# Kernel optimization log

Measured on AMD Instinct MI355X. Metric: run time of the kernel, lower is better.

The kernel has to match this reference:

```python
import jax, jax.numpy as jnp
import numpy as np

OPS_SIZE = (40, 40, 40)
ALPHA = 0.005
BETA = 0.01


def _disp_from_landmarks(coords, values):
    # coords, values: (N,3). Returns (3, W0, H0, D0) coarse displacement field.
    D0, H0, W0 = OPS_SIZE
    axes = [jnp.linspace(-1.0, 1.0, s) for s in OPS_SIZE]
    grid = jnp.stack(jnp.meshgrid(*axes, indexing='ij'), -1).reshape(-1, 3)  # (G,3)
    # squared distance ||g - c||^2 via expansion (avoids (N,G,3) repeat tensor)
    d2 = (jnp.sum(grid * grid, -1)[:, None]
          + jnp.sum(coords * coords, -1)[None, :]
          - 2.0 * grid @ coords.T)  # (G,N)
    w = jnp.exp(-d2 / ALPHA)
    w = (BETA + 1.0) * w / (jnp.sum(w, axis=1, keepdims=True) + BETA)
    disp = (w @ values).reshape(D0, H0, W0, 3)
    return jnp.transpose(disp, (3, 2, 1, 0))  # torch permute(3,2,1,0)


def _interp_axis(x, axis, out_s):
    # 1D linear resize along `axis`, matching F.interpolate align_corners=False
    in_s = x.shape[axis]
    c = jnp.maximum((jnp.arange(out_s, dtype=jnp.float32) + 0.5) * (in_s / out_s) - 0.5, 0.0)
    i0 = jnp.minimum(jnp.floor(c).astype(jnp.int32), in_s - 1)
    i1 = jnp.minimum(i0 + 1, in_s - 1)
    t = (c - i0.astype(jnp.float32)).astype(x.dtype)
    shp = [1] * x.ndim
    shp[axis] = out_s
    t = t.reshape(shp)
    return jnp.take(x, i0, axis=axis) * (1 - t) + jnp.take(x, i1, axis=axis) * t


def _resize_trilinear(x, out_size):
    # x: (C, d, h, w) -> (C, D, H, W); trilinear resize is separable
    for ax, s in zip((1, 2, 3), out_size):
        x = _interp_axis(x, ax, s)
    return x


def _grid_sample_3d(vol, grid):
    # vol: (B,C,D,H,W), grid: (B,Do,Ho,Wo,3), grid[...,0]=x indexes W.
    # mode='bilinear' (trilinear), padding_mode='zeros', align_corners=False
    B, C, D, H, W = vol.shape
    x = ((grid[..., 0] + 1.0) * W - 1.0) / 2.0
    y = ((grid[..., 1] + 1.0) * H - 1.0) / 2.0
    z = ((grid[..., 2] + 1.0) * D - 1.0) / 2.0

    def per_batch(v, x, y, z):
        x0 = jnp.floor(x); y0 = jnp.floor(y); z0 = jnp.floor(z)
        fx = x - x0; fy = y - y0; fz = z - z0
        x0i = x0.astype(jnp.int32); y0i = y0.astype(jnp.int32); z0i = z0.astype(jnp.int32)
        acc = jnp.zeros((C,) + x.shape, v.dtype)
        for dz in (0, 1):
            wz = fz if dz else 1.0 - fz
            zi = z0i + dz
            for dy in (0, 1):
                wy = fy if dy else 1.0 - fy
                yi = y0i + dy
                for dx in (0, 1):
                    wx = fx if dx else 1.0 - fx
                    xi = x0i + dx
                    m = ((zi >= 0) & (zi < D) & (yi >= 0) & (yi < H) & (xi >= 0) & (xi < W)).astype(v.dtype)
                    zc = jnp.clip(zi, 0, D - 1); yc = jnp.clip(yi, 0, H - 1); xc = jnp.clip(xi, 0, W - 1)
                    acc = acc + v[:, zc, yc, xc] * ((wz * wy * wx * m)[None])
        return acc

    return jax.vmap(per_batch)(vol, x, y, z)


def reference(orgin_mask, control_points_coords, control_points_offsets):
    B, C, D, H, W = orgin_mask.shape
    coords = control_points_coords + control_points_offsets  # (B,N,3)
    vals = -control_points_offsets                            # (B,N,3)
    disp = jax.vmap(_disp_from_landmarks)(coords, vals)       # (B,3,W0,H0,D0)
    flow = jax.vmap(lambda d: _resize_trilinear(d, (D, H, W)))(disp)  # (B,3,D,H,W)
    axes = [jnp.linspace(-1.0, 1.0, s) for s in (D, H, W)]
    base = jnp.stack(jnp.meshgrid(*axes, indexing='ij'), 0)   # (3,D,H,W)
    base = jnp.transpose(base, (0, 3, 2, 1))                  # torch permute(0,1,4,3,2); needs D==H==W
    warped = base[None] + flow                                # (B,3,D,H,W)
    warped = jnp.transpose(warped, (0, 2, 3, 4, 1))           # (B,D,H,W,3)
    return _grid_sample_3d(orgin_mask, warped)


def setup_inputs() -> dict:
    key = jax.random.key(0)
    k1, k2, k3 = jax.random.split(key, 3)
    orgin_mask = jax.random.uniform(k1, (2, 1, 128, 128, 128), dtype=jnp.float32)
    control_points_coords = jax.random.uniform(k2, (2, 1024, 3), dtype=jnp.float32, minval=-1.0, maxval=1.0)
    control_points_offsets = jax.random.normal(k3, (2, 1024, 3), dtype=jnp.float32) * 0.05
    return {"orgin_mask": orgin_mask,
            "control_points_coords": control_points_coords,
            "control_points_offsets": control_points_offsets}
```

## Files before the change

kernel.cpp:

```cpp
#include <hip/hip_runtime.h>
#include <math.h>

#define NLM   1024
#define NB    2
#define OPS   40
#define DIM   128
#define OPS3  (OPS*OPS*OPS)
#define DIM3  (DIM*DIM*DIM)

#define P_T 4
#define Q_T 4
#define R_T 8
#define NP  (OPS/P_T)
#define NQ  (OPS/Q_T)
#define NR  (OPS/R_T)
#define MARGIN 0.30f

#define K2f  (-288.5390081777927f)
#define M2f  ( 577.0780163555854f)


__device__ __forceinline__ float fexp2(float x) {
#if __has_builtin(__builtin_amdgcn_exp2f)
    return __builtin_amdgcn_exp2f(x);
#else
    return exp2f(x);
#endif
}

__global__ __launch_bounds__(128)
void coarse_kernel(const float* __restrict__ coords, const float* __restrict__ offs,
                   float4* __restrict__ C) {
    __shared__ float4 sA[NLM];
    __shared__ float4 sV[NLM];
    __shared__ int sCnt;

    const int t = threadIdx.x;
    const int b = blockIdx.y;
    const int tile = blockIdx.x;
    const int tp = tile / (NQ*NR);
    const int tq = (tile / NR) % NQ;
    const int tr = tile % NR;

    const float step = 2.f / (OPS - 1);
    const float bx0 = -1.f + step * (tr*R_T)          - MARGIN;
    const float bx1 = -1.f + step * (tr*R_T + R_T-1)  + MARGIN;
    const float by0 = -1.f + step * (tq*Q_T)          - MARGIN;
    const float by1 = -1.f + step * (tq*Q_T + Q_T-1)  + MARGIN;
    const float bz0 = -1.f + step * (tp*P_T)          - MARGIN;
    const float bz1 = -1.f + step * (tp*P_T + P_T-1)  + MARGIN;

    if (t == 0) sCnt = 0;
    __syncthreads();

    for (int n = t; n < NLM; n += 128) {
        const float* cp = coords + (b*NLM + n)*3;
        const float* op = offs   + (b*NLM + n)*3;
        float ox = op[0], oy = op[1], oz = op[2];
        float cx = cp[0] + ox, cy = cp[1] + oy, cz = cp[2] + oz;
        if (cx >= bx0 && cx <= bx1 && cy >= by0 && cy <= by1 &&
            cz >= bz0 && cz <= bz1) {
            int idx = atomicAdd(&sCnt, 1);
            sA[idx] = make_float4(cx, cy, cz, K2f*(cx*cx + cy*cy + cz*cz));
            sV[idx] = make_float4(-ox, -oy, -oz, 0.f);
        }
    }
    __syncthreads();
    const int cnt = sCnt;

    const int lp = t >> 5;
    const int lq = (t >> 3) & 3;
    const int lr = t & 7;
    const float gx = -1.f + step * (tr*R_T + lr);
    const float gy = -1.f + step * (tq*Q_T + lq);
    const float gz = -1.f + step * (tp*P_T + lp);
    const float h  = K2f * (gx*gx + gy*gy + gz*gz);

    float aS = 0.f, aX = 0.f, aY = 0.f, aZ = 0.f;
    for (int n = 0; n < cnt; ++n) {
        float4 a = sA[n];
        float4 v = sV[n];
        float u   = fmaf(gx, a.x, fmaf(gy, a.y, gz*a.z));
        float arg = fmaf(M2f, u, h + a.w);
        float e   = fexp2(arg);
        aS += e;
        aX = fmaf(e, v.x, aX);
        aY = fmaf(e, v.y, aY);
        aZ = fmaf(e, v.z, aZ);
    }

    const int p = tp*P_T + lp, q = tq*Q_T + lq, r = tr*R_T + lr;
    const float inv = 1.01f / (aS + 0.01f);
    C[b*OPS3 + (p*OPS + q)*OPS + r] = make_float4(aX*inv, aY*inv, aZ*inv, 0.f);
}

__device__ __forceinline__ void axis_interp(int t, int& a0, int& a1, float& w) {
    float c = fmaxf(0.3125f * (float)t - 0.34375f, 0.f);
    float f = floorf(c);
    a0 = (int)f;
    a1 = min(a0 + 1, OPS - 1);
    w = c - f;
}

__device__ __forceinline__ float4 lerp4(float4 a, float4 b, float t) {
    return make_float4(a.x + t*(b.x - a.x),
                       a.y + t*(b.y - a.y),
                       a.z + t*(b.z - a.z),
                       0.f);
}

typedef float vf2 __attribute__((ext_vector_type(2)));
struct __attribute__((packed, aligned(4))) P2 { vf2 v; };
__device__ __forceinline__ vf2 load2(const float* p) {
    return ((const P2*)p)->v;
}

struct AW {
    int r0, r1, r2, r3, xs;
    float e0, e1, wy0, wy1, wz0, wz1;
};

__device__ __forceinline__ AW make_aw(float px, float py, float pz) {
    AW s;
    float xf = floorf(px), yf = floorf(py), zf = floorf(pz);
    int x0 = (int)xf, y0 = (int)yf, z0 = (int)zf;
    float ax = px - xf, ay = py - yf, az = pz - zf;

    float wx0 = ((unsigned)x0     < 128u) ? (1.f - ax) : 0.f;
    float wx1 = ((unsigned)(x0+1) < 128u) ? ax         : 0.f;
    s.wy0 = ((unsigned)y0     < 128u) ? (1.f - ay) : 0.f;
    s.wy1 = ((unsigned)(y0+1) < 128u) ? ay         : 0.f;
    s.wz0 = ((unsigned)z0     < 128u) ? (1.f - az) : 0.f;
    s.wz1 = ((unsigned)(z0+1) < 128u) ? az         : 0.f;

    s.xs = min(max(x0, 0), 126);
    int d = x0 - s.xs;
    s.e0 = (d == 0) ? wx0 : ((d == -1) ? wx1 : 0.f);
    s.e1 = (d == 0) ? wx1 : ((d ==  1) ? wx0 : 0.f);

    int ya = (y0 & 127) << 7, yb2 = ((y0+1) & 127) << 7;
    int za = (z0 & 127) << 14, zb2 = ((z0+1) & 127) << 14;
    s.r0 = za + ya;  s.r1 = za + yb2;
    s.r2 = zb2 + ya; s.r3 = zb2 + yb2;
    return s;
}

__global__ __launch_bounds__(256)
void warp_kernel(const float* __restrict__ mask, const float4* __restrict__ C,
                 float* __restrict__ out) {
    __shared__ float4 sF[4][OPS];

    const int g = blockIdx.x;
    const int w = threadIdx.x >> 6;
    const int lane = threadIdx.x & 63;
    const int line = ((g & 7) << 12) + ((g >> 3) << 2) + w;
    const int j = line & (DIM-1);
    const int i = (line >> 7) & (DIM-1);
    const int b = line >> 14;

    int i0,i1,j0,j1; float ti,tj;
    axis_interp(i, i0, i1, ti);
    axis_interp(j, j0, j1, tj);

    const float4* Cb = C + b*OPS3;
    if (lane < OPS) {
        float4 c00 = Cb[(i0*OPS + j0)*OPS + lane];
        float4 c01 = Cb[(i0*OPS + j1)*OPS + lane];
        float4 c10 = Cb[(i1*OPS + j0)*OPS + lane];
        float4 c11 = Cb[(i1*OPS + j1)*OPS + lane];
        sF[w][lane] = lerp4(lerp4(c00, c01, tj), lerp4(c10, c11, tj), ti);
    }

    const float* M = mask + b * DIM3;
    const float s127 = 2.f / (DIM - 1);
    const float yb = -1.f + s127 * (float)j;
    const float zb = -1.f + s127 * (float)i;

    AW aw[2];
    #pragma unroll
    for (int c = 0; c < 2; ++c) {
        const int k = lane + (c << 6);
        int k0,k1; float tk;
        axis_interp(k, k0, k1, tk);
        float4 fl = lerp4(sF[w][k0], sF[w][k1], tk);
        float x = -1.f + s127 * (float)k + fl.x;
        float y = yb + fl.y;
        float z = zb + fl.z;
        aw[c] = make_aw(((x + 1.f) * (float)DIM - 1.f) * 0.5f,
                        ((y + 1.f) * (float)DIM - 1.f) * 0.5f,
                        ((z + 1.f) * (float)DIM - 1.f) * 0.5f);
    }

    vf2 t0[4], t1[4];
    {
        const AW& s = aw[0];
        t0[0] = load2(M + s.r0 + s.xs);
        t0[1] = load2(M + s.r1 + s.xs);
        t0[2] = load2(M + s.r2 + s.xs);
        t0[3] = load2(M + s.r3 + s.xs);
    }
    {
        const AW& s = aw[1];
        t1[0] = load2(M + s.r0 + s.xs);
        t1[1] = load2(M + s.r1 + s.xs);
        t1[2] = load2(M + s.r2 + s.xs);
        t1[3] = load2(M + s.r3 + s.xs);
    }

    float res[2];
    #pragma unroll
    for (int c = 0; c < 2; ++c) {
        const AW& s = aw[c];
        const vf2* tv = c ? t1 : t0;
        float w00 = s.wz0*s.wy0, w01 = s.wz0*s.wy1;
        float w10 = s.wz1*s.wy0, w11 = s.wz1*s.wy1;
        float r;
        r = tv[0].x * (w00*s.e0);
        r = fmaf(tv[0].y, w00*s.e1, r);
        r = fmaf(tv[1].x, w01*s.e0, r);
        r = fmaf(tv[1].y, w01*s.e1, r);
        r = fmaf(tv[2].x, w10*s.e0, r);
        r = fmaf(tv[2].y, w10*s.e1, r);
        r = fmaf(tv[3].x, w11*s.e0, r);
        r = fmaf(tv[3].y, w11*s.e1, r);
        res[c] = r;
    }
    out[(line << 7) + lane]      = res[0];
    out[(line << 7) + lane + 64] = res[1];
}

extern "C" void kernel_launch(void* const* d_in, const int* in_sizes, int n_in,
                              void* d_out, int out_size, void* d_ws, size_t ws_size,
                              hipStream_t stream) {
    const float* mask   = (const float*)d_in[0];
    const float* coords = (const float*)d_in[1];
    const float* offs   = (const float*)d_in[2];
    float* out = (float*)d_out;

    float4* coarse = (float4*)d_ws;

    dim3 g1(NP*NQ*NR, NB);
    coarse_kernel<<<g1, 128, 0, stream>>>(coords, offs, coarse);

    warp_kernel<<<NB*DIM*DIM/4, 256, 0, stream>>>(mask, coarse, out);
}
```

Measured before the change: 97.98 us.

## Stage per-wave bounding box of mask rows in LDS before trilinear gather

For each half-line, the wave reduces its min/max z, y and x sample indices with shuffles. If the bounding box fits, it copies those mask rows into shared memory with coalesced loads and gathers the eight corners from LDS. Otherwise it falls back to direct global gathers. The goal is to replace scattered 8-byte global loads with coalesced row copies, at the cost of wave reductions, extra LDS traffic and a serial copy loop.

Result: slower. 123.9 us (+26.5%).

```diff
diff --git a/kernel.cpp b/kernel.cpp
--- a/kernel.cpp
+++ b/kernel.cpp
@@ -18,6 +18,9 @@
 
 #define K2f  (-288.5390081777927f)
 #define M2f  ( 577.0780163555854f)
+
+#define ROWS_MAX 20
+#define NX_MAX   96
 
 
 __device__ __forceinline__ float fexp2(float x) {
@@ -116,7 +119,7 @@
 }
 
 struct AW {
-    int r0, r1, r2, r3, xs;
+    int za, zb, ya, yb, xs;
     float e0, e1, wy0, wy1, wz0, wz1;
 };
 
@@ -138,17 +141,45 @@
     s.e0 = (d == 0) ? wx0 : ((d == -1) ? wx1 : 0.f);
     s.e1 = (d == 0) ? wx1 : ((d ==  1) ? wx0 : 0.f);
 
-    int ya = (y0 & 127) << 7, yb2 = ((y0+1) & 127) << 7;
-    int za = (z0 & 127) << 14, zb2 = ((z0+1) & 127) << 14;
-    s.r0 = za + ya;  s.r1 = za + yb2;
-    s.r2 = zb2 + ya; s.r3 = zb2 + yb2;
+    s.ya = min(max(y0,   0), 127);
+    s.yb = min(max(y0+1, 0), 127);
+    s.za = min(max(z0,   0), 127);
+    s.zb = min(max(z0+1, 0), 127);
     return s;
+}
+
+__device__ __forceinline__ int wave_min(int v) {
+    #pragma unroll
+    for (int m = 32; m; m >>= 1) v = min(v, __shfl_xor(v, m, 64));
+    return v;
+}
+__device__ __forceinline__ int wave_max(int v) {
+    #pragma unroll
+    for (int m = 32; m; m >>= 1) v = max(v, __shfl_xor(v, m, 64));
+    return v;
+}
+
+__device__ __forceinline__ float accum8(float a0, float a1, float b0, float b1,
+                                        float c0, float c1, float d0, float d1,
+                                        const AW& s) {
+    float w00 = s.wz0*s.wy0, w01 = s.wz0*s.wy1;
+    float w10 = s.wz1*s.wy0, w11 = s.wz1*s.wy1;
+    float r = a0 * (w00*s.e0);
+    r = fmaf(a1, w00*s.e1, r);
+    r = fmaf(b0, w01*s.e0, r);
+    r = fmaf(b1, w01*s.e1, r);
+    r = fmaf(c0, w10*s.e0, r);
+    r = fmaf(c1, w10*s.e1, r);
+    r = fmaf(d0, w11*s.e0, r);
+    r = fmaf(d1, w11*s.e1, r);
+    return r;
 }
 
 __global__ __launch_bounds__(256)
 void warp_kernel(const float* __restrict__ mask, const float4* __restrict__ C,
                  float* __restrict__ out) {
     __shared__ float4 sF[4][OPS];
+    __shared__ float sTile[4][ROWS_MAX*NX_MAX];
 
     const int g = blockIdx.x;
     const int w = threadIdx.x >> 6;
@@ -173,10 +204,10 @@
 
     const float* M = mask + b * DIM3;
     const float s127 = 2.f / (DIM - 1);
-    const float yb = -1.f + s127 * (float)j;
-    const float zb = -1.f + s127 * (float)i;
-
-    AW aw[2];
+    const float yb2 = -1.f + s127 * (float)j;
+    const float zb2 = -1.f + s127 * (float)i;
+
+    float res[2];
     #pragma unroll
     for (int c = 0; c < 2; ++c) {
         const int k = lane + (c << 6);
@@ -184,47 +215,50 @@
         axis_interp(k, k0, k1, tk);
         float4 fl = lerp4(sF[w][k0], sF[w][k1], tk);
         float x = -1.f + s127 * (float)k + fl.x;
-        float y = yb + fl.y;
-        float z = zb + fl.z;
-        aw[c] = make_aw(((x + 1.f) * (float)DIM - 1.f) * 0.5f,
-                        ((y + 1.f) * (float)DIM - 1.f) * 0.5f,
-                        ((z + 1.f) * (float)DIM - 1.f) * 0.5f);
-    }
-
-    vf2 t0[4], t1[4];
-    {
-        const AW& s = aw[0];
-        t0[0] = load2(M + s.r0 + s.xs);
-        t0[1] = load2(M + s.r1 + s.xs);
-        t0[2] = load2(M + s.r2 + s.xs);
-        t0[3] = load2(M + s.r3 + s.xs);
-    }
-    {
-        const AW& s = aw[1];
-        t1[0] = load2(M + s.r0 + s.xs);
-        t1[1] = load2(M + s.r1 + s.xs);
-        t1[2] = load2(M + s.r2 + s.xs);
-        t1[3] = load2(M + s.r3 + s.xs);
-    }
-
-    float res[2];
-    #pragma unroll
-    for (int c = 0; c < 2; ++c) {
-        const AW& s = aw[c];
-        const vf2* tv = c ? t1 : t0;
-        float w00 = s.wz0*s.wy0, w01 = s.wz0*s.wy1;
-        float w10 = s.wz1*s.wy0, w11 = s.wz1*s.wy1;
-        float r;
-        r = tv[0].x * (w00*s.e0);
-        r = fmaf(tv[0].y, w00*s.e1, r);
-        r = fmaf(tv[1].x, w01*s.e0, r);
-        r = fmaf(tv[1].y, w01*s.e1, r);
-        r = fmaf(tv[2].x, w10*s.e0, r);
-        r = fmaf(tv[2].y, w10*s.e1, r);
-        r = fmaf(tv[3].x, w11*s.e0, r);
-        r = fmaf(tv[3].y, w11*s.e1, r);
-        res[c] = r;
-    }
+        float y = yb2 + fl.y;
+        float z = zb2 + fl.z;
+        AW s = make_aw(((x + 1.f) * (float)DIM - 1.f) * 0.5f,
+                       ((y + 1.f) * (float)DIM - 1.f) * 0.5f,
+                       ((z + 1.f) * (float)DIM - 1.f) * 0.5f);
+
+        const int minZ = wave_min(s.za), maxZ = wave_max(s.zb);
+        const int minY = wave_min(s.ya), maxY = wave_max(s.yb);
+        const int minX = wave_min(s.xs), maxX = wave_max(s.xs);
+        const int nz = maxZ - minZ + 1;
+        const int ny = maxY - minY + 1;
+        const int nx = maxX - minX + 2;
+
+        if (nz*ny <= ROWS_MAX && nx <= NX_MAX) {
+            float* T = sTile[w];
+            int row = 0;
+            for (int zz = minZ; zz <= maxZ; ++zz) {
+                for (int yy = minY; yy <= maxY; ++yy, ++row) {
+                    const float* src = M + (zz << 14) + (yy << 7) + minX;
+                    float* dst = T + row*NX_MAX;
+                    for (int xx = lane; xx < nx; xx += 64)
+                        dst[xx] = src[xx];
+                }
+            }
+            const int xl = s.xs - minX;
+            const float* p00 = T + ((s.za - minZ)*ny + (s.ya - minY))*NX_MAX + xl;
+            const float* p01 = T + ((s.za - minZ)*ny + (s.yb - minY))*NX_MAX + xl;
+            const float* p10 = T + ((s.zb - minZ)*ny + (s.ya - minY))*NX_MAX + xl;
+            const float* p11 = T + ((s.zb - minZ)*ny + (s.yb - minY))*NX_MAX + xl;
+            res[c] = accum8(p00[0], p00[1], p01[0], p01[1],
+                            p10[0], p10[1], p11[0], p11[1], s);
+        } else {
+            const int r0 = (s.za << 14) + (s.ya << 7);
+            const int r1 = (s.za << 14) + (s.yb << 7);
+            const int r2 = (s.zb << 14) + (s.ya << 7);
+            const int r3 = (s.zb << 14) + (s.yb << 7);
+            vf2 t0 = load2(M + r0 + s.xs);
+            vf2 t1 = load2(M + r1 + s.xs);
+            vf2 t2 = load2(M + r2 + s.xs);
+            vf2 t3 = load2(M + r3 + s.xs);
+            res[c] = accum8(t0.x, t0.y, t1.x, t1.y, t2.x, t2.y, t3.x, t3.y, s);
+        }
+    }
+
     out[(line << 7) + lane]      = res[0];
     out[(line << 7) + lane + 64] = res[1];
 }
```
